# Performance work log

Measured on AMD Instinct MI355X. Metric: run time of the kernel, lower is better.

The kernel has to match this reference:

```python
import jax, jax.numpy as jnp
import numpy as np
import math

B, S, D_MODEL, H = 2, 2048, 1024, 16
HD = D_MODEL // H  # head_dim = 64


def _rope(x, seq_len):
    # x: [B, S, H, HD]; standard rotate-half RoPE with base 10000
    d = x.shape[-1]
    inv_freq = 1.0 / (10000.0 ** (jnp.arange(0, d, 2, dtype=jnp.float32) / d))
    t = jnp.arange(seq_len, dtype=jnp.float32)
    freqs = t[:, None] * inv_freq[None, :]              # [S, HD/2]
    emb = jnp.concatenate([freqs, freqs], axis=-1)      # [S, HD]
    cos = jnp.cos(emb)[None, :, None, :]
    sin = jnp.sin(emb)[None, :, None, :]
    x1, x2 = jnp.split(x, 2, axis=-1)
    rot = jnp.concatenate([-x2, x1], axis=-1)
    return x * cos + rot * sin


def setup_inputs() -> dict:
    key = jax.random.key(0)
    ks = jax.random.split(key, 11)
    s = 1.0 / math.sqrt(D_MODEL)
    return {
        "query": jax.random.normal(ks[0], (B, S, D_MODEL), jnp.float32),
        "keys": jax.random.normal(ks[1], (B, S, D_MODEL), jnp.float32),
        "values": jax.random.normal(ks[2], (B, S, D_MODEL), jnp.float32),
        "Wq": jax.random.normal(ks[3], (D_MODEL, D_MODEL), jnp.float32) * s,
        "bq": jnp.zeros((D_MODEL,), jnp.float32),
        "Wk": jax.random.normal(ks[4], (D_MODEL, D_MODEL), jnp.float32) * s,
        "bk": jnp.zeros((D_MODEL,), jnp.float32),
        "Wv": jax.random.normal(ks[5], (D_MODEL, D_MODEL), jnp.float32) * s,
        "bv": jnp.zeros((D_MODEL,), jnp.float32),
        "Wo": jax.random.normal(ks[6], (D_MODEL, D_MODEL), jnp.float32) * s,
        "bo": jnp.zeros((D_MODEL,), jnp.float32),
    }


def reference(query, keys, values, Wq, bq, Wk, bk, Wv, bv, Wo, bo):
    b, s, _ = query.shape
    scale = math.sqrt(HD)
    q = (query @ Wq.T + bq).reshape(b, s, H, HD)   # [B,S,H,HD]
    k = (keys @ Wk.T + bk).reshape(b, s, H, HD)
    v = (values @ Wv.T + bv).reshape(b, s, H, HD)
    q = _rope(q, s)
    k = _rope(k, s)
    # scores: [B,H,Sq,Sk]
    scores = jnp.einsum('bqhd,bkhd->bhqk', q, k)
    causal = jnp.tril(jnp.ones((s, s), dtype=bool))[None, None]
    scores = jnp.where(causal, scores, -jnp.inf) / scale
    attn = jax.nn.softmax(scores, axis=-1)
    ctx = jnp.einsum('bhqk,bkhd->bqhd', attn, v).reshape(b, s, H * HD)
    out = ctx @ Wo.T + bo
    return out, attn
```

## Files before the change

### kernel.cpp

```cpp
#include <hip/hip_runtime.h>
#include <hip/hip_bf16.h>
#include <stdint.h>
#include <math.h>


typedef __attribute__((ext_vector_type(8))) __bf16 bf16x8;
typedef __attribute__((ext_vector_type(4))) float f32x4;

__device__ __forceinline__ unsigned short f2bf(float f) {
  unsigned int u = __float_as_uint(f);
  u += 0x7fffu + ((u >> 16) & 1u);
  return (unsigned short)(u >> 16);
}

typedef const __attribute__((address_space(1))) unsigned int* gas_ptr;
typedef __attribute__((address_space(3))) unsigned int* las_ptr;
__device__ __forceinline__ void glds16(const void* g, void* l) {
  __builtin_amdgcn_global_load_lds((gas_ptr)g, (las_ptr)l, 16, 0, 0);
}

__global__ __launch_bounds__(256) void rope_table(float2* __restrict__ tab) {
  const int i = blockIdx.x * 256 + threadIdx.x;
  const int spos = i >> 5, d = i & 31;
  const double invf = pow(10000.0, -(double)d / 32.0);
  const double ang = (double)spos * invf;
  double sn, cs;
  sincos(ang, &sn, &cs);
  tab[i] = make_float2((float)cs, (float)sn);
}

__global__ __launch_bounds__(256) void cvt_all(
    const float* __restrict__ a0, const float* __restrict__ a1,
    const float* __restrict__ a2, const float* __restrict__ w0,
    const float* __restrict__ w1, const float* __restrict__ w2,
    const float* __restrict__ w3, unsigned short* __restrict__ ws) {
  const int z = blockIdx.z;
  const float* src;
  unsigned short* dst;
  int n;
  if (z == 0)      { src = a0; dst = ws;             n = 4194304; }
  else if (z == 1) { src = a1; dst = ws + 4194304;   n = 4194304; }
  else if (z == 2) { src = a2; dst = ws + 8388608;   n = 4194304; }
  else if (z == 3) { src = w0; dst = ws + 12582912;  n = 1048576; }
  else if (z == 4) { src = w1; dst = ws + 13631488;  n = 1048576; }
  else if (z == 5) { src = w2; dst = ws + 14680064;  n = 1048576; }
  else             { src = w3; dst = ws + 15728640;  n = 1048576; }
  const int n4 = n >> 2;
  for (int i = blockIdx.x * 256 + threadIdx.x; i < n4; i += gridDim.x * 256) {
    float4 f = ((const float4*)src)[i];
    ushort4 u;
    u.x = f2bf(f.x); u.y = f2bf(f.y); u.z = f2bf(f.z); u.w = f2bf(f.w);
    ((ushort4*)dst)[i] = u;
  }
}

__global__ __launch_bounds__(256) void gemm_qkv(
    const unsigned short* __restrict__ xq, const unsigned short* __restrict__ xk,
    const unsigned short* __restrict__ xv, const unsigned short* __restrict__ wq,
    const unsigned short* __restrict__ wk, const unsigned short* __restrict__ wv,
    const float* __restrict__ bq, const float* __restrict__ bk,
    const float* __restrict__ bv, const float2* __restrict__ rtab,
    unsigned short* __restrict__ qo, unsigned short* __restrict__ ko,
    unsigned short* __restrict__ vo) {
  const int z = blockIdx.z;
  const unsigned short* A = (z == 0) ? xq : (z == 1) ? xk : xv;
  const unsigned short* W = (z == 0) ? wq : (z == 1) ? wk : wv;
  const float* bias = (z == 0) ? bq : (z == 1) ? bk : bv;
  unsigned short* out = (z == 0) ? qo : (z == 1) ? ko : vo;

  const int t = threadIdx.x;
  const int lane = t & 63, wave = t >> 6;
  const int wr = wave >> 1, wc = wave & 1;
  const int lrow = lane & 15, lkb = lane >> 4;
  const int m0 = blockIdx.y * 128, n0 = blockIdx.x * 128;

  __shared__ __align__(16) unsigned short abuf[4096];
  __shared__ __align__(16) unsigned short bbuf[4096];

  f32x4 acc[4][4] = {};

  for (int k0 = 0; k0 < 1024; k0 += 32) {
    __syncthreads();
#pragma unroll
    for (int i = 0; i < 2; ++i) {
      int slot = i * 256 + t;
      int kb = slot >> 7, row = slot & 127;
      glds16(A + (size_t)(m0 + row) * 1024 + k0 + kb * 8, &abuf[slot * 8]);
      glds16(W + (size_t)(n0 + row) * 1024 + k0 + kb * 8, &bbuf[slot * 8]);
    }
    __syncthreads();
    bf16x8 af[4], bfr[4];
#pragma unroll
    for (int mi = 0; mi < 4; ++mi)
      af[mi] = *(const bf16x8*)&abuf[(lkb * 128 + wr * 64 + mi * 16 + lrow) * 8];
#pragma unroll
    for (int ni = 0; ni < 4; ++ni)
      bfr[ni] = *(const bf16x8*)&bbuf[(lkb * 128 + wc * 64 + ni * 16 + lrow) * 8];
#pragma unroll
    for (int mi = 0; mi < 4; ++mi)
#pragma unroll
      for (int ni = 0; ni < 4; ++ni)
        acc[mi][ni] = __builtin_amdgcn_mfma_f32_16x16x32_bf16(af[mi], bfr[ni],
                                                              acc[mi][ni], 0, 0, 0);
  }

  const int nbase = n0 + wc * 64;
  float bias_v[4];
#pragma unroll
  for (int ni = 0; ni < 4; ++ni) bias_v[ni] = bias[nbase + ni * 16 + lrow];

  const int mbase = m0 + wr * 64 + 4 * lkb;
  const bool rope = (z < 2);
  const float qsc = (z == 0) ? 0.125f : 1.0f;

#pragma unroll
  for (int mi = 0; mi < 4; ++mi) {
#pragma unroll
    for (int r = 0; r < 4; ++r) {
      const int m = mbase + mi * 16 + r;
      const int bidx = m >> 11, spos = m & 2047;
      float vals[4];
#pragma unroll
      for (int ni = 0; ni < 4; ++ni) vals[ni] = acc[mi][ni][r] + bias_v[ni];
      if (rope) {
#pragma unroll
        for (int ni = 0; ni < 2; ++ni) {
          const int d = ni * 16 + lrow;
          const float2 cs2 = rtab[spos * 32 + d];
          float x1 = vals[ni], x2 = vals[ni + 2];
          vals[ni] = (x1 * cs2.x - x2 * cs2.y) * qsc;
          vals[ni + 2] = (x2 * cs2.x + x1 * cs2.y) * qsc;
        }
      }
#pragma unroll
      for (int ni = 0; ni < 4; ++ni) {
        const int n = nbase + ni * 16 + lrow;
        const int h = n >> 6, d = n & 63;
        out[(size_t)((bidx * 16 + h) * 2048 + spos) * 64 + d] = f2bf(vals[ni]);
      }
    }
  }
}

__global__ __launch_bounds__(256) void gemm_out(
    const unsigned short* __restrict__ A, const unsigned short* __restrict__ W,
    const float* __restrict__ bias, float* __restrict__ out) {
  const int t = threadIdx.x;
  const int lane = t & 63, wave = t >> 6;
  const int wr = wave >> 1, wc = wave & 1;
  const int lrow = lane & 15, lkb = lane >> 4;
  const int m0 = blockIdx.y * 128, n0 = blockIdx.x * 128;

  __shared__ __align__(16) unsigned short abuf[4096];
  __shared__ __align__(16) unsigned short bbuf[4096];

  f32x4 acc[4][4] = {};

  for (int k0 = 0; k0 < 1024; k0 += 32) {
    __syncthreads();
#pragma unroll
    for (int i = 0; i < 2; ++i) {
      int slot = i * 256 + t;
      int kb = slot >> 7, row = slot & 127;
      glds16(A + (size_t)(m0 + row) * 1024 + k0 + kb * 8, &abuf[slot * 8]);
      glds16(W + (size_t)(n0 + row) * 1024 + k0 + kb * 8, &bbuf[slot * 8]);
    }
    __syncthreads();
    bf16x8 af[4], bfr[4];
#pragma unroll
    for (int mi = 0; mi < 4; ++mi)
      af[mi] = *(const bf16x8*)&abuf[(lkb * 128 + wr * 64 + mi * 16 + lrow) * 8];
#pragma unroll
    for (int ni = 0; ni < 4; ++ni)
      bfr[ni] = *(const bf16x8*)&bbuf[(lkb * 128 + wc * 64 + ni * 16 + lrow) * 8];
#pragma unroll
    for (int mi = 0; mi < 4; ++mi)
#pragma unroll
      for (int ni = 0; ni < 4; ++ni)
        acc[mi][ni] = __builtin_amdgcn_mfma_f32_16x16x32_bf16(af[mi], bfr[ni],
                                                              acc[mi][ni], 0, 0, 0);
  }

  const int nbase = n0 + wc * 64;
  float bias_v[4];
#pragma unroll
  for (int ni = 0; ni < 4; ++ni) bias_v[ni] = bias[nbase + ni * 16 + lrow];
  const int mbase = m0 + wr * 64 + 4 * lkb;
#pragma unroll
  for (int mi = 0; mi < 4; ++mi)
#pragma unroll
    for (int r = 0; r < 4; ++r) {
      const int m = mbase + mi * 16 + r;
      float* orow = out + (size_t)m * 1024 + nbase;
#pragma unroll
      for (int ni = 0; ni < 4; ++ni)
        orow[ni * 16 + lrow] = acc[mi][ni][r] + bias_v[ni];
    }
}

__global__ __launch_bounds__(256) void transpose_v(
    const unsigned short* __restrict__ v, unsigned short* __restrict__ vt) {
  const int s0 = blockIdx.x * 64;
  const int bh = blockIdx.y;
  __shared__ __align__(16) unsigned short tile[64][80];
  const int t = threadIdx.x;
  {
    const int row = t >> 2, cb = t & 3;
    const unsigned short* src = v + (size_t)(bh * 2048 + s0 + row) * 64 + cb * 16;
    *(uint4*)&tile[row][cb * 16] = *(const uint4*)src;
    *(uint4*)&tile[row][cb * 16 + 8] = *(const uint4*)(src + 8);
  }
  __syncthreads();
  {
    const int d = t >> 2, sc = t & 3;
    __align__(16) unsigned short tmp[16];
#pragma unroll
    for (int u = 0; u < 16; ++u) tmp[u] = tile[sc * 16 + u][d];
    unsigned short* dst = vt + (size_t)(bh * 64 + d) * 2048 + s0 + sc * 16;
    *(uint4*)dst = *(const uint4*)&tmp[0];
    *(uint4*)(dst + 8) = *(const uint4*)&tmp[8];
  }
}

__global__ __launch_bounds__(256) void attn_kernel(
    const unsigned short* __restrict__ Q, const unsigned short* __restrict__ Km,
    const unsigned short* __restrict__ Vt, float* __restrict__ attn,
    unsigned short* __restrict__ ctx) {
  const int p = blockIdx.x;
  const int qta = p, qtb = 31 - p;
  const int bh = blockIdx.y;
  const int t = threadIdx.x;
  const int lane = t & 63, wave = t >> 6;
  const int lrow = lane & 15, lg = lane >> 4;
  const int wq0a = qta * 64 + wave * 16;
  const int wq0b = qtb * 64 + wave * 16;

  const unsigned short* Qb = Q + (size_t)bh * 2048 * 64;
  const unsigned short* Kb = Km + (size_t)bh * 2048 * 64;
  const unsigned short* Vb = Vt + (size_t)bh * 64 * 2048;
  float* attn_b = attn + (size_t)bh * 2048 * 2048;

  __shared__ __align__(16) unsigned short kbuf[4096];
  __shared__ __align__(16) unsigned short vbuf[4096];
  __shared__ __align__(16) unsigned short pbuf[4][1024];

  bf16x8 qfa[2], qfb[2];
#pragma unroll
  for (int dk = 0; dk < 2; ++dk) {
    qfa[dk] = *(const bf16x8*)(Qb + (size_t)(wq0a + lrow) * 64 + dk * 32 + lg * 8);
    qfb[dk] = *(const bf16x8*)(Qb + (size_t)(wq0b + lrow) * 64 + dk * 32 + lg * 8);
  }

  float l_a[4] = {0.f, 0.f, 0.f, 0.f};
  float l_b[4] = {0.f, 0.f, 0.f, 0.f};

  auto lupdate = [&](const unsigned short* buf, int kbase, int wq0,
                     const bf16x8* qf, float* l_loc) {
    f32x4 s[4] = {};
#pragma unroll
    for (int fc = 0; fc < 4; ++fc)
#pragma unroll
      for (int dk = 0; dk < 2; ++dk) {
        bf16x8 kf = *(const bf16x8*)&buf[((dk * 4 + lg) * 64 + fc * 16 + lrow) * 8];
        s[fc] = __builtin_amdgcn_mfma_f32_16x16x32_bf16(qf[dk], kf, s[fc], 0, 0, 0);
      }
#pragma unroll
    for (int r = 0; r < 4; ++r) {
      const int qg = wq0 + 4 * lg + r;
      float sum = 0.f;
#pragma unroll
      for (int fc = 0; fc < 4; ++fc) {
        const int kg = kbase + fc * 16 + lrow;
        sum += __expf((kg <= qg) ? s[fc][r] : -1e30f);
      }
      l_loc[r] += sum;
    }
  };

  for (int kt = 0; kt <= qtb; kt += 2) {
    const int k0 = kt * 64;
    const bool two = (kt + 1) <= qtb;
    __syncthreads();
#pragma unroll
    for (int i = 0; i < 2; ++i) {
      int slot = i * 256 + t;
      int cb = slot >> 6, row = slot & 63;
      glds16(Kb + (size_t)(k0 + row) * 64 + cb * 8, &kbuf[slot * 8]);
      if (two)
        glds16(Kb + (size_t)(k0 + 64 + row) * 64 + cb * 8, &vbuf[slot * 8]);
    }
    __syncthreads();
    if (kt <= qta) lupdate(kbuf, k0, wq0a, qfa, l_a);
    lupdate(kbuf, k0, wq0b, qfb, l_b);
    if (two) {
      if (kt + 1 <= qta) lupdate(vbuf, k0 + 64, wq0a, qfa, l_a);
      lupdate(vbuf, k0 + 64, wq0b, qfb, l_b);
    }
  }

  float loglinva[4], loglinvb[4];
#pragma unroll
  for (int r = 0; r < 4; ++r) {
    float la = l_a[r], lb = l_b[r];
#pragma unroll
    for (int off = 1; off < 16; off <<= 1) {
      la += __shfl_xor(la, off);
      lb += __shfl_xor(lb, off);
    }
    loglinva[r] = -__logf(la);
    loglinvb[r] = -__logf(lb);
  }

  f32x4 oaa[4] = {};
  f32x4 oab[4] = {};

  auto process = [&](int k0, int wq0, const bf16x8* qf, const float* loglinv,
                     f32x4* oa) {
    f32x4 s[4] = {};
#pragma unroll
    for (int fc = 0; fc < 4; ++fc)
#pragma unroll
      for (int dk = 0; dk < 2; ++dk) {
        bf16x8 kf = *(const bf16x8*)&kbuf[((dk * 4 + lg) * 64 + fc * 16 + lrow) * 8];
        s[fc] = __builtin_amdgcn_mfma_f32_16x16x32_bf16(qf[dk], kf, s[fc], 0, 0, 0);
      }
#pragma unroll
    for (int r = 0; r < 4; ++r) {
      const int qg = wq0 + 4 * lg + r;
      const int q_ = 4 * lg + r;
      float* arow = attn_b + (size_t)qg * 2048 + k0;
#pragma unroll
      for (int fc = 0; fc < 4; ++fc) {
        const int kg = k0 + fc * 16 + lrow;
        const float pv = (kg <= qg) ? __expf(s[fc][r] + loglinv[r]) : 0.f;
        arow[fc * 16 + lrow] = pv;
        const int k_ = fc * 16 + lrow;
        const int dl = q_ + 16 * ((k_ >> 3) & 3);
        const int kk = k_ >> 5, j = k_ & 7;
        int byteo = (kk * 64 + dl) * 16 + j * 2;
        byteo ^= ((kk * 8 + (dl >> 3)) & 7) << 4;
        *(unsigned short*)((char*)pbuf[wave] + byteo) = f2bf(pv);
      }
    }
#pragma unroll
    for (int kk = 0; kk < 2; ++kk) {
      int rbyte = (kk * 64 + lane) * 16;
      rbyte ^= ((kk * 8 + (lane >> 3)) & 7) << 4;
      bf16x8 pa = *(const bf16x8*)((char*)pbuf[wave] + rbyte);
#pragma unroll
      for (int fd = 0; fd < 4; ++fd) {
        bf16x8 vf = *(const bf16x8*)&vbuf[((kk * 4 + lg) * 64 + fd * 16 + lrow) * 8];
        oa[fd] = __builtin_amdgcn_mfma_f32_16x16x32_bf16(pa, vf, oa[fd], 0, 0, 0);
      }
    }
  };

  for (int kt = 0; kt <= qtb; ++kt) {
    const int k0 = kt * 64;
    __syncthreads();
#pragma unroll
    for (int i = 0; i < 2; ++i) {
      int slot = i * 256 + t;
      int cb = slot >> 6, row = slot & 63;
      glds16(Kb + (size_t)(k0 + row) * 64 + cb * 8, &kbuf[slot * 8]);
      glds16(Vb + (size_t)row * 2048 + k0 + cb * 8, &vbuf[slot * 8]);
    }
    __syncthreads();
    if (kt <= qta) process(k0, wq0a, qfa, loglinva, oaa);
    process(k0, wq0b, qfb, loglinvb, oab);
  }

  {
    const int zc0a = (qta + 1) * 16;
    for (int rr = 0; rr < 16; ++rr) {
      float4* arow = (float4*)(attn_b + (size_t)(wq0a + rr) * 2048);
      for (int c = zc0a + lane; c < 512; c += 64)
        arow[c] = make_float4(0.f, 0.f, 0.f, 0.f);
    }
    const int zc0b = (qtb + 1) * 16;
    for (int rr = 0; rr < 16; ++rr) {
      float4* arow = (float4*)(attn_b + (size_t)(wq0b + rr) * 2048);
      for (int c = zc0b + lane; c < 512; c += 64)
        arow[c] = make_float4(0.f, 0.f, 0.f, 0.f);
    }
  }

  const int bidx = bh >> 4, h = bh & 15;
#pragma unroll
  for (int fd = 0; fd < 4; ++fd)
#pragma unroll
    for (int r = 0; r < 4; ++r) {
      const int qga = wq0a + 4 * lg + r;
      const int qgb = wq0b + 4 * lg + r;
      ctx[(size_t)(bidx * 2048 + qga) * 1024 + h * 64 + fd * 16 + lrow] =
          f2bf(oaa[fd][r]);
      ctx[(size_t)(bidx * 2048 + qgb) * 1024 + h * 64 + fd * 16 + lrow] =
          f2bf(oab[fd][r]);
    }
}

extern "C" void kernel_launch(void* const* d_in, const int* in_sizes, int n_in,
                              void* d_out, int out_size, void* d_ws, size_t ws_size,
                              hipStream_t stream) {
  const float* q_in = (const float*)d_in[0];
  const float* k_in = (const float*)d_in[1];
  const float* v_in = (const float*)d_in[2];
  const float* Wq = (const float*)d_in[3];
  const float* bq = (const float*)d_in[4];
  const float* Wk = (const float*)d_in[5];
  const float* bk = (const float*)d_in[6];
  const float* Wv = (const float*)d_in[7];
  const float* bv = (const float*)d_in[8];
  const float* Wo = (const float*)d_in[9];
  const float* bo = (const float*)d_in[10];

  unsigned short* ws = (unsigned short*)d_ws;
  float* outp = (float*)d_out;

  const size_t OXQ = 0, OXK = 4194304, OXV = 8388608;
  const size_t OWQ = 12582912, OWK = 13631488, OWV = 14680064, OWO = 15728640;
  const size_t OQ = 16777216, OK = 20971520, OV = 25165824;
  const size_t OTAB = 29360128;
  const size_t OVT = OXK;
  const size_t OCTX = OXQ;
  float2* rtab = (float2*)(ws + OTAB);

  rope_table<<<dim3(256), 256, 0, stream>>>(rtab);
  cvt_all<<<dim3(512, 1, 7), 256, 0, stream>>>(q_in, k_in, v_in, Wq, Wk, Wv, Wo, ws);
  gemm_qkv<<<dim3(8, 32, 3), 256, 0, stream>>>(ws + OXQ, ws + OXK, ws + OXV,
                                               ws + OWQ, ws + OWK, ws + OWV,
                                               bq, bk, bv, rtab,
                                               ws + OQ, ws + OK, ws + OV);
  transpose_v<<<dim3(32, 32), 256, 0, stream>>>(ws + OV, ws + OVT);
  attn_kernel<<<dim3(16, 32), 256, 0, stream>>>(ws + OQ, ws + OK, ws + OVT,
                                                outp + 4194304, ws + OCTX);
  gemm_out<<<dim3(8, 32), 256, 0, stream>>>(ws + OCTX, ws + OWO, bo, outp);
}
```

Measured before the change: 318.7 us.

## Transpose score MFMA so each lane owns one query row, vectorizing attn stores

Swaps the MFMA operand order so the score tile is computed as K×Q, putting each lane on a single query row with four consecutive keys. The attn probabilities can then be written as float4 stores instead of scattered scalar stores, and the row-sum needs only two cross-lane shuffles with a single log per lane. The P staging buffer moves to a padded row-major layout (stride 68) written as ushort4, replacing the XOR-swizzled scalar writes. The padding may leave some LDS bank conflicts on the bf16x8 reads.

```diff
diff --git a/kernel.cpp b/kernel.cpp
--- a/kernel.cpp
+++ b/kernel.cpp
@@ -242,7 +242,7 @@
 
   __shared__ __align__(16) unsigned short kbuf[4096];
   __shared__ __align__(16) unsigned short vbuf[4096];
-  __shared__ __align__(16) unsigned short pbuf[4][1024];
+  __shared__ __align__(16) unsigned short pbuf[4][16 * 68];
 
   bf16x8 qfa[2], qfb[2];
 #pragma unroll
@@ -251,30 +251,28 @@
     qfb[dk] = *(const bf16x8*)(Qb + (size_t)(wq0b + lrow) * 64 + dk * 32 + lg * 8);
   }
 
-  float l_a[4] = {0.f, 0.f, 0.f, 0.f};
-  float l_b[4] = {0.f, 0.f, 0.f, 0.f};
+  float l_a = 0.f, l_b = 0.f;
 
   auto lupdate = [&](const unsigned short* buf, int kbase, int wq0,
-                     const bf16x8* qf, float* l_loc) {
+                     const bf16x8* qf, float& l_loc) {
     f32x4 s[4] = {};
 #pragma unroll
     for (int fc = 0; fc < 4; ++fc)
 #pragma unroll
       for (int dk = 0; dk < 2; ++dk) {
         bf16x8 kf = *(const bf16x8*)&buf[((dk * 4 + lg) * 64 + fc * 16 + lrow) * 8];
-        s[fc] = __builtin_amdgcn_mfma_f32_16x16x32_bf16(qf[dk], kf, s[fc], 0, 0, 0);
-      }
-#pragma unroll
-    for (int r = 0; r < 4; ++r) {
-      const int qg = wq0 + 4 * lg + r;
-      float sum = 0.f;
-#pragma unroll
-      for (int fc = 0; fc < 4; ++fc) {
-        const int kg = kbase + fc * 16 + lrow;
+        s[fc] = __builtin_amdgcn_mfma_f32_16x16x32_bf16(kf, qf[dk], s[fc], 0, 0, 0);
+      }
+    const int qg = wq0 + lrow;
+    float sum = 0.f;
+#pragma unroll
+    for (int fc = 0; fc < 4; ++fc)
+#pragma unroll
+      for (int r = 0; r < 4; ++r) {
+        const int kg = kbase + fc * 16 + 4 * lg + r;
         sum += __expf((kg <= qg) ? s[fc][r] : -1e30f);
       }
-      l_loc[r] += sum;
-    }
+    l_loc += sum;
   };
 
   for (int kt = 0; kt <= qtb; kt += 2) {
@@ -298,23 +296,16 @@
     }
   }
 
-  float loglinva[4], loglinvb[4];
-#pragma unroll
-  for (int r = 0; r < 4; ++r) {
-    float la = l_a[r], lb = l_b[r];
-#pragma unroll
-    for (int off = 1; off < 16; off <<= 1) {
-      la += __shfl_xor(la, off);
-      lb += __shfl_xor(lb, off);
-    }
-    loglinva[r] = -__logf(la);
-    loglinvb[r] = -__logf(lb);
-  }
+  l_a += __shfl_xor(l_a, 16); l_a += __shfl_xor(l_a, 32);
+  l_b += __shfl_xor(l_b, 16); l_b += __shfl_xor(l_b, 32);
+  const float loglinva = -__logf(l_a);
+  const float loglinvb = -__logf(l_b);
 
   f32x4 oaa[4] = {};
   f32x4 oab[4] = {};
-
-  auto process = [&](int k0, int wq0, const bf16x8* qf, const float* loglinv,
+  unsigned short* plds = pbuf[wave];
+
+  auto process = [&](int k0, int wq0, const bf16x8* qf, float loglinv,
                      f32x4* oa) {
     f32x4 s[4] = {};
 #pragma unroll
@@ -322,31 +313,27 @@
 #pragma unroll
       for (int dk = 0; dk < 2; ++dk) {
         bf16x8 kf = *(const bf16x8*)&kbuf[((dk * 4 + lg) * 64 + fc * 16 + lrow) * 8];
-        s[fc] = __builtin_amdgcn_mfma_f32_16x16x32_bf16(qf[dk], kf, s[fc], 0, 0, 0);
-      }
-#pragma unroll
-    for (int r = 0; r < 4; ++r) {
-      const int qg = wq0 + 4 * lg + r;
-      const int q_ = 4 * lg + r;
-      float* arow = attn_b + (size_t)qg * 2048 + k0;
-#pragma unroll
-      for (int fc = 0; fc < 4; ++fc) {
-        const int kg = k0 + fc * 16 + lrow;
-        const float pv = (kg <= qg) ? __expf(s[fc][r] + loglinv[r]) : 0.f;
-        arow[fc * 16 + lrow] = pv;
-        const int k_ = fc * 16 + lrow;
-        const int dl = q_ + 16 * ((k_ >> 3) & 3);
-        const int kk = k_ >> 5, j = k_ & 7;
-        int byteo = (kk * 64 + dl) * 16 + j * 2;
-        byteo ^= ((kk * 8 + (dl >> 3)) & 7) << 4;
-        *(unsigned short*)((char*)pbuf[wave] + byteo) = f2bf(pv);
-      }
+        s[fc] = __builtin_amdgcn_mfma_f32_16x16x32_bf16(kf, qf[dk], s[fc], 0, 0, 0);
+      }
+    const int qg = wq0 + lrow;
+    float* arow = attn_b + (size_t)qg * 2048 + k0 + 4 * lg;
+#pragma unroll
+    for (int fc = 0; fc < 4; ++fc) {
+      const int kg0 = k0 + fc * 16 + 4 * lg;
+      float4 pv4;
+      pv4.x = __expf((kg0 + 0 <= qg) ? s[fc][0] + loglinv : -1e30f);
+      pv4.y = __expf((kg0 + 1 <= qg) ? s[fc][1] + loglinv : -1e30f);
+      pv4.z = __expf((kg0 + 2 <= qg) ? s[fc][2] + loglinv : -1e30f);
+      pv4.w = __expf((kg0 + 3 <= qg) ? s[fc][3] + loglinv : -1e30f);
+      *(float4*)(arow + fc * 16) = pv4;
+      ushort4 pb;
+      pb.x = f2bf(pv4.x); pb.y = f2bf(pv4.y);
+      pb.z = f2bf(pv4.z); pb.w = f2bf(pv4.w);
+      *(ushort4*)&plds[lrow * 68 + fc * 16 + 4 * lg] = pb;
     }
 #pragma unroll
     for (int kk = 0; kk < 2; ++kk) {
-      int rbyte = (kk * 64 + lane) * 16;
-      rbyte ^= ((kk * 8 + (lane >> 3)) & 7) << 4;
-      bf16x8 pa = *(const bf16x8*)((char*)pbuf[wave] + rbyte);
+      bf16x8 pa = *(const bf16x8*)&plds[lrow * 68 + kk * 32 + lg * 8];
 #pragma unroll
       for (int fd = 0; fd < 4; ++fd) {
         bf16x8 vf = *(const bf16x8*)&vbuf[((kk * 4 + lg) * 64 + fd * 16 + lrow) * 8];
```

Result: slower. 327.2 us (+2.7%).
